# Kernel optimization log

Measured on AMD Instinct MI355X. Metric: run time of the kernel, lower is better.

## Reference

```python
import jax, jax.numpy as jnp
import numpy as np

B, T, C, H = 4, 2048, 1024, 16
D = C // H  # head_dim = 64

def setup_inputs() -> dict:
    key = jax.random.key(0)
    k1, k2, k3 = jax.random.split(key, 3)
    x = jax.random.normal(k1, (B, T, C), dtype=jnp.float32)
    w_qkv = jax.random.normal(k2, (C, 3 * C), dtype=jnp.float32) * (C ** -0.5)
    w_proj = jax.random.normal(k3, (C, C), dtype=jnp.float32) * (C ** -0.5)
    b_proj = jnp.zeros((C,), dtype=jnp.float32)
    return {"x": x, "w_qkv": w_qkv, "w_proj": w_proj, "b_proj": b_proj}

def reference(x, w_qkv, w_proj, b_proj):
    Bx, Tx, Cx = x.shape
    qkv = x @ w_qkv  # [B,T,3C]
    q, k, v = jnp.split(qkv, 3, axis=-1)
    # [B,T,H,D] -> [B,H,T,D]
    q = q.reshape(Bx, Tx, H, D).transpose(0, 2, 1, 3)
    k = k.reshape(Bx, Tx, H, D).transpose(0, 2, 1, 3)
    v = v.reshape(Bx, Tx, H, D).transpose(0, 2, 1, 3)
    scale = 1.0 / np.sqrt(D).astype(np.float32)
    att = jnp.einsum('bhqd,bhkd->bhqk', q, k) * scale  # [B,H,T,T]
    causal = jnp.tril(jnp.ones((Tx, Tx), dtype=bool))
    att = jnp.where(causal, att, -jnp.inf)
    att = jax.nn.softmax(att, axis=-1)
    y = jnp.einsum('bhqk,bhkd->bhqd', att, v)  # [B,H,T,D]
    y = y.transpose(0, 2, 1, 3).reshape(Bx, Tx, Cx)
    return y @ w_proj + b_proj
```

## Files before the change

### kernel.cpp

```cpp
#include <hip/hip_runtime.h>

typedef unsigned short u16;
typedef unsigned int u32;
typedef __attribute__((ext_vector_type(8))) short bf16x8;
typedef __attribute__((ext_vector_type(4))) float f32x4;
typedef __attribute__((ext_vector_type(16))) float f32x16;
typedef __attribute__((ext_vector_type(4))) unsigned short u16x4;

#define MFMA16(a, b, c) __builtin_amdgcn_mfma_f32_16x16x32_bf16((a), (b), (c), 0, 0, 0)
#define MFMA32(a, b, c) __builtin_amdgcn_mfma_f32_32x32x16_bf16((a), (b), (c), 0, 0, 0)

__device__ __forceinline__ u16 f2bf(float f) {
  union { float f; unsigned int i; } v; v.f = f;
  return (u16)((v.i + 0x7FFFu + ((v.i >> 16) & 1u)) >> 16);
}
__device__ __forceinline__ float exp2a(float x) {
  float r; asm("v_exp_f32 %0, %1" : "=v"(r) : "v"(x)); return r;
}
__device__ __forceinline__ u32 cvtpk(float lo, float hi) {
  u32 d; asm("v_cvt_pk_bf16_f32 %0, %1, %2" : "=v"(d) : "v"(lo), "v"(hi)); return d;
}
__device__ __forceinline__ void gl2lds16(const u16* g, u16* l) {
  __builtin_amdgcn_global_load_lds(
      (const __attribute__((address_space(1))) void*)g,
      (__attribute__((address_space(3))) void*)l, 16, 0, 0);
}

__global__ __launch_bounds__(256) void k_ingest(const float* __restrict__ src,
                                                u16* __restrict__ dst, int n8) {
  const int i = blockIdx.x * 256 + threadIdx.x;
  if (i >= n8) return;
  const float* s = src + (size_t)i * 8;
  float4 a = *(const float4*)(s);
  float4 b = *(const float4*)(s + 4);
  union { u16 o[8]; int4 v; } u;
  u.o[0] = f2bf(a.x); u.o[1] = f2bf(a.y); u.o[2] = f2bf(a.z); u.o[3] = f2bf(a.w);
  u.o[4] = f2bf(b.x); u.o[5] = f2bf(b.y); u.o[6] = f2bf(b.z); u.o[7] = f2bf(b.w);
  *(int4*)(&dst[(size_t)i * 8]) = u.v;
}

__global__ __launch_bounds__(256) void k_transpose(const float* __restrict__ src,
                                                   u16* __restrict__ dst, int R, int C) {
  __shared__ u16 tile[64][65];
  const int c0 = blockIdx.x * 64, r0 = blockIdx.y * 64;
  const int t = threadIdx.x;
#pragma unroll
  for (int i = 0; i < 16; ++i) {
    int e = i * 256 + t, rr = e >> 6, cc = e & 63;
    tile[rr][cc] = f2bf(src[(size_t)(r0 + rr) * C + c0 + cc]);
  }
  __syncthreads();
#pragma unroll
  for (int i = 0; i < 16; ++i) {
    int e = i * 256 + t, rr = e >> 6, cc = e & 63;
    dst[(size_t)(c0 + rr) * R + r0 + cc] = tile[cc][rr];
  }
}

template <int QKV>
__global__ __launch_bounds__(256) void k_gemm(
    const u16* __restrict__ A, const u16* __restrict__ Bt,
    const float* __restrict__ bias, float* __restrict__ Cf,
    u16* __restrict__ Qb, u16* __restrict__ Kb, u16* __restrict__ VTb,
    int M, int N, int K) {
  __shared__ __attribute__((aligned(16))) u16 As[128 * 32];
  __shared__ __attribute__((aligned(16))) u16 Bs[128 * 32];
  const int bn = blockIdx.x, bm = blockIdx.y;
  const int t = threadIdx.x, lane = t & 63, w = t >> 6;
  const int wr = w >> 1, wc = w & 1;
  const int rh = lane & 15, kg = lane >> 4;
  const int srow = lane >> 2, sk8 = (lane & 3) << 3;

  f32x4 acc[4][4];
#pragma unroll
  for (int mi = 0; mi < 4; ++mi)
#pragma unroll
    for (int ni = 0; ni < 4; ++ni) acc[mi][ni] = (f32x4)0.0f;

  for (int k0 = 0; k0 < K; k0 += 32) {
#pragma unroll
    for (int i = 0; i < 2; ++i) {
      const int r0 = w * 32 + i * 16;
      gl2lds16(&A[(size_t)(bm * 128 + r0 + srow) * K + k0 + sk8], &As[r0 * 32]);
      gl2lds16(&Bt[(size_t)(bn * 128 + r0 + srow) * K + k0 + sk8], &Bs[r0 * 32]);
    }
    asm volatile("s_waitcnt vmcnt(0)" ::: "memory");
    __syncthreads();

    bf16x8 af[4], bfr[4];
#pragma unroll
    for (int mi = 0; mi < 4; ++mi)
      af[mi] = *(const bf16x8*)(&As[(wr * 64 + mi * 16 + rh) * 32 + kg * 8]);
#pragma unroll
    for (int ni = 0; ni < 4; ++ni)
      bfr[ni] = *(const bf16x8*)(&Bs[(wc * 64 + ni * 16 + rh) * 32 + kg * 8]);
    __builtin_amdgcn_s_setprio(1);
#pragma unroll
    for (int mi = 0; mi < 4; ++mi)
#pragma unroll
      for (int ni = 0; ni < 4; ++ni)
        acc[mi][ni] = MFMA16(af[mi], bfr[ni], acc[mi][ni]);
    __builtin_amdgcn_s_setprio(0);
    __syncthreads();
  }

  if (QKV == 0) {
    const int rbase = bm * 128 + wr * 64;
    const int cbase = bn * 128 + wc * 64;
#pragma unroll
    for (int ni = 0; ni < 4; ++ni) {
      const int col = cbase + ni * 16 + rh;
      const float bv = bias ? bias[col] : 0.0f;
#pragma unroll
      for (int mi = 0; mi < 4; ++mi) {
#pragma unroll
        for (int r = 0; r < 4; ++r) {
          int row = rbase + mi * 16 + kg * 4 + r;
          Cf[(size_t)row * N + col] = acc[mi][ni][r] + bv;
        }
      }
    }
  } else {
    const float SCQ = 0.125f * 1.44269504f;
    const int rowbase = bm * 128 + wr * 64;
    const int b = rowbase >> 11;
    const int tb = rowbase & 2047;
    const int cbase = bn * 128 + wc * 64;
    const int role = cbase >> 10;
    const int h = (cbase & 1023) >> 6;
    const int bh = b * 16 + h;
#pragma unroll
    for (int ni = 0; ni < 4; ++ni) {
      const int d = ni * 16 + rh;
#pragma unroll
      for (int mi = 0; mi < 4; ++mi) {
        const int tt = tb + mi * 16 + kg * 4;
        if (role == 2) {
          u16x4 pk;
#pragma unroll
          for (int r = 0; r < 4; ++r) pk[r] = f2bf(acc[mi][ni][r]);
          *(u16x4*)(&VTb[((size_t)bh * 64 + d) * 2048 + tt]) = pk;
        } else {
          u16* dst = (role == 0) ? Qb : Kb;
          const float sc = (role == 0) ? SCQ : 1.0f;
#pragma unroll
          for (int r = 0; r < 4; ++r)
            dst[((size_t)bh * 2048 + tt + r) * 64 + d] = f2bf(acc[mi][ni][r] * sc);
        }
      }
    }
  }
}

__global__ __launch_bounds__(128, 2) void k_attn(const u16* __restrict__ Qb,
                                                 const u16* __restrict__ Kb,
                                                 const u16* __restrict__ VTb,
                                                 u16* __restrict__ Y) {
  const int bh = blockIdx.x;
  const int w = threadIdx.x >> 6;
  const int sb = w ? 31 - (int)blockIdx.y : (int)blockIdx.y;
  const int lane = threadIdx.x & 63;
  const int q31 = lane & 31, hi = lane >> 5;
  const int qA = sb * 64 + q31;
  const int qBr = sb * 64 + 32 + q31;
  const u16* Qh = Qb + (size_t)bh * 2048 * 64;
  const u16* Kh = Kb + (size_t)bh * 2048 * 64;
  const u16* Vh = VTb + (size_t)bh * 64 * 2048;
  const int b = bh >> 4, h = bh & 15;

  bf16x8 qfA[4], qfB[4];
#pragma unroll
  for (int d = 0; d < 4; ++d) {
    qfA[d] = *(const bf16x8*)(&Qh[(size_t)qA * 64 + d * 16 + hi * 8]);
    qfB[d] = *(const bf16x8*)(&Qh[(size_t)qBr * 64 + d * 16 + hi * 8]);
  }

  f32x16 oA0 = (f32x16)0.0f, oA1 = (f32x16)0.0f;
  f32x16 oB0 = (f32x16)0.0f, oB1 = (f32x16)0.0f;
  float mA = -1e30f, sA = 0.0f, mB = -1e30f, sB = 0.0f;

  const int nt = 2 * sb + 2;
  for (int tt = 0; tt < nt; ++tt) {
    const int j0 = tt * 32;
    const bool aAct = tt < nt - 1;

    bf16x8 kf[4];
#pragma unroll
    for (int d = 0; d < 4; ++d)
      kf[d] = *(const bf16x8*)(&Kh[(size_t)(j0 + q31) * 64 + d * 16 + hi * 8]);
    const bf16x8 vf0 = *(const bf16x8*)(&Vh[(size_t)q31 * 2048 + j0 + hi * 8]);
    const bf16x8 vf1 = *(const bf16x8*)(&Vh[(size_t)q31 * 2048 + j0 + 16 + hi * 8]);
    const bf16x8 vf2 = *(const bf16x8*)(&Vh[(size_t)(32 + q31) * 2048 + j0 + hi * 8]);
    const bf16x8 vf3 = *(const bf16x8*)(&Vh[(size_t)(32 + q31) * 2048 + j0 + 16 + hi * 8]);

    f32x16 stB = (f32x16)0.0f;
    __builtin_amdgcn_s_setprio(1);
#pragma unroll
    for (int d = 0; d < 4; ++d) stB = MFMA32(kf[d], qfB[d], stB);
    f32x16 stA = (f32x16)0.0f;
    if (aAct) {
#pragma unroll
      for (int d = 0; d < 4; ++d) stA = MFMA32(kf[d], qfA[d], stA);
    }
    __builtin_amdgcn_s_setprio(0);

    if (tt == nt - 2) {
#pragma unroll
      for (int r = 0; r < 16; ++r) {
        const int kcol = (r & 3) + 8 * (r >> 2) + 4 * hi;
        if (kcol > q31) stA[r] = -1e30f;
      }
    }
    if (tt == nt - 1) {
#pragma unroll
      for (int r = 0; r < 16; ++r) {
        const int kcol = (r & 3) + 8 * (r >> 2) + 4 * hi;
        if (kcol > q31) stB[r] = -1e30f;
      }
    }

    union { u32 w4[4]; bf16x8 f; } paA0, paA1, paB0, paB1;
    if (aAct) {
      float mx = fmaxf(
          fmaxf(fmaxf(fmaxf(stA[0], stA[1]), fmaxf(stA[2], stA[3])),
                fmaxf(fmaxf(stA[4], stA[5]), fmaxf(stA[6], stA[7]))),
          fmaxf(fmaxf(fmaxf(stA[8], stA[9]), fmaxf(stA[10], stA[11])),
                fmaxf(fmaxf(stA[12], stA[13]), fmaxf(stA[14], stA[15]))));
      if (__any(mx - mA > 8.0f)) {
        mx = fmaxf(mx, __shfl_xor(mx, 32));
        const float mn = fmaxf(mA, mx);
        const float scf = exp2a(mA - mn);
        mA = mn; sA *= scf; oA0 *= scf; oA1 *= scf;
      }
      float p[16];
#pragma unroll
      for (int r = 0; r < 16; ++r) p[r] = exp2a(stA[r] - mA);
      sA += (((p[0] + p[1]) + (p[2] + p[3])) + ((p[4] + p[5]) + (p[6] + p[7]))) +
            (((p[8] + p[9]) + (p[10] + p[11])) + ((p[12] + p[13]) + (p[14] + p[15])));
      u32 D0 = cvtpk(p[0], p[1]),   D1 = cvtpk(p[2], p[3]);
      u32 D2 = cvtpk(p[4], p[5]),   D3 = cvtpk(p[6], p[7]);
      u32 D4 = cvtpk(p[8], p[9]),   D5 = cvtpk(p[10], p[11]);
      u32 D6 = cvtpk(p[12], p[13]), D7 = cvtpk(p[14], p[15]);
      u32 X0 = __shfl_xor(D0, 32), X1 = __shfl_xor(D1, 32);
      u32 X2 = __shfl_xor(D2, 32), X3 = __shfl_xor(D3, 32);
      u32 X4 = __shfl_xor(D4, 32), X5 = __shfl_xor(D5, 32);
      u32 X6 = __shfl_xor(D6, 32), X7 = __shfl_xor(D7, 32);
      paA0.w4[0] = hi ? X2 : D0; paA0.w4[1] = hi ? X3 : D1;
      paA0.w4[2] = hi ? D2 : X0; paA0.w4[3] = hi ? D3 : X1;
      paA1.w4[0] = hi ? X6 : D4; paA1.w4[1] = hi ? X7 : D5;
      paA1.w4[2] = hi ? D6 : X4; paA1.w4[3] = hi ? D7 : X5;
    }

    {
      float mx = fmaxf(
          fmaxf(fmaxf(fmaxf(stB[0], stB[1]), fmaxf(stB[2], stB[3])),
                fmaxf(fmaxf(stB[4], stB[5]), fmaxf(stB[6], stB[7]))),
          fmaxf(fmaxf(fmaxf(stB[8], stB[9]), fmaxf(stB[10], stB[11])),
                fmaxf(fmaxf(stB[12], stB[13]), fmaxf(stB[14], stB[15]))));
      if (__any(mx - mB > 8.0f)) {
        mx = fmaxf(mx, __shfl_xor(mx, 32));
        const float mn = fmaxf(mB, mx);
        const float scf = exp2a(mB - mn);
        mB = mn; sB *= scf; oB0 *= scf; oB1 *= scf;
      }
      float p[16];
#pragma unroll
      for (int r = 0; r < 16; ++r) p[r] = exp2a(stB[r] - mB);
      sB += (((p[0] + p[1]) + (p[2] + p[3])) + ((p[4] + p[5]) + (p[6] + p[7]))) +
            (((p[8] + p[9]) + (p[10] + p[11])) + ((p[12] + p[13]) + (p[14] + p[15])));
      u32 D0 = cvtpk(p[0], p[1]),   D1 = cvtpk(p[2], p[3]);
      u32 D2 = cvtpk(p[4], p[5]),   D3 = cvtpk(p[6], p[7]);
      u32 D4 = cvtpk(p[8], p[9]),   D5 = cvtpk(p[10], p[11]);
      u32 D6 = cvtpk(p[12], p[13]), D7 = cvtpk(p[14], p[15]);
      u32 X0 = __shfl_xor(D0, 32), X1 = __shfl_xor(D1, 32);
      u32 X2 = __shfl_xor(D2, 32), X3 = __shfl_xor(D3, 32);
      u32 X4 = __shfl_xor(D4, 32), X5 = __shfl_xor(D5, 32);
      u32 X6 = __shfl_xor(D6, 32), X7 = __shfl_xor(D7, 32);
      paB0.w4[0] = hi ? X2 : D0; paB0.w4[1] = hi ? X3 : D1;
      paB0.w4[2] = hi ? D2 : X0; paB0.w4[3] = hi ? D3 : X1;
      paB1.w4[0] = hi ? X6 : D4; paB1.w4[1] = hi ? X7 : D5;
      paB1.w4[2] = hi ? D6 : X4; paB1.w4[3] = hi ? D7 : X5;
    }

    __builtin_amdgcn_s_setprio(1);
    oB0 = MFMA32(vf0, paB0.f, oB0);
    oB0 = MFMA32(vf1, paB1.f, oB0);
    oB1 = MFMA32(vf2, paB0.f, oB1);
    oB1 = MFMA32(vf3, paB1.f, oB1);
    if (aAct) {
      oA0 = MFMA32(vf0, paA0.f, oA0);
      oA0 = MFMA32(vf1, paA1.f, oA0);
      oA1 = MFMA32(vf2, paA0.f, oA1);
      oA1 = MFMA32(vf3, paA1.f, oA1);
    }
    __builtin_amdgcn_s_setprio(0);
  }

  sA += __shfl_xor(sA, 32);
  sB += __shfl_xor(sB, 32);
  const float invA = 1.0f / sA, invB = 1.0f / sB;
  u16* yrowA = Y + ((size_t)b * 2048 + qA) * 1024 + h * 64;
  u16* yrowB = Y + ((size_t)b * 2048 + qBr) * 1024 + h * 64;
#pragma unroll
  for (int a = 0; a < 4; ++a) {
    u16x4 pk;
#pragma unroll
    for (int i = 0; i < 4; ++i) pk[i] = f2bf(oA0[a * 4 + i] * invA);
    *(u16x4*)(yrowA + a * 8 + 4 * hi) = pk;
#pragma unroll
    for (int i = 0; i < 4; ++i) pk[i] = f2bf(oA1[a * 4 + i] * invA);
    *(u16x4*)(yrowA + 32 + a * 8 + 4 * hi) = pk;
#pragma unroll
    for (int i = 0; i < 4; ++i) pk[i] = f2bf(oB0[a * 4 + i] * invB);
    *(u16x4*)(yrowB + a * 8 + 4 * hi) = pk;
#pragma unroll
    for (int i = 0; i < 4; ++i) pk[i] = f2bf(oB1[a * 4 + i] * invB);
    *(u16x4*)(yrowB + 32 + a * 8 + 4 * hi) = pk;
  }
}

extern "C" void kernel_launch(void* const* d_in, const int* in_sizes, int n_in,
                              void* d_out, int out_size, void* d_ws, size_t ws_size,
                              hipStream_t stream) {
  const float* x      = (const float*)d_in[0];
  const float* w_qkv  = (const float*)d_in[1];
  const float* w_proj = (const float*)d_in[2];
  const float* b_proj = (const float*)d_in[3];
  float* out = (float*)d_out;

  char* ws = (char*)d_ws;
  u16* wqkvT  = (u16*)(ws);
  u16* wprojT = (u16*)(ws + 6291456);
  u16* Qb     = (u16*)(ws + 8388608);
  u16* Kb     = (u16*)(ws + 25165824);
  u16* VTb    = (u16*)(ws + 41943040);
  u16* xb     = (u16*)(ws + 58720256);
  u16* Yb     = xb;

  k_ingest<<<4096, 256, 0, stream>>>(x, xb, 1048576);
  k_transpose<<<dim3(48, 16), 256, 0, stream>>>(w_qkv, wqkvT, 1024, 3072);
  k_transpose<<<dim3(16, 16), 256, 0, stream>>>(w_proj, wprojT, 1024, 1024);
  k_gemm<1><<<dim3(24, 64), 256, 0, stream>>>(xb, wqkvT, nullptr, nullptr,
                                              Qb, Kb, VTb, 8192, 3072, 1024);
  k_attn<<<dim3(64, 16), 128, 0, stream>>>(Qb, Kb, VTb, Yb);
  k_gemm<0><<<dim3(8, 64), 256, 0, stream>>>(Yb, wprojT, b_proj, out,
                                             nullptr, nullptr, nullptr, 8192, 1024, 1024);
}
```

Measured before the change: 212.9 us.

## Split attention KV loop across two waves with LDS softmax merge

```diff
diff --git a/kernel.cpp b/kernel.cpp
--- a/kernel.cpp
+++ b/kernel.cpp
@@ -152,13 +152,14 @@
   }
 }
 
-__global__ __launch_bounds__(128, 2) void k_attn(const u16* __restrict__ Qb,
+__global__ __launch_bounds__(128, 4) void k_attn(const u16* __restrict__ Qb,
                                                  const u16* __restrict__ Kb,
                                                  const u16* __restrict__ VTb,
                                                  u16* __restrict__ Y) {
+  __shared__ float MG[64][68];
   const int bh = blockIdx.x;
+  const int sb = 31 - (int)blockIdx.y;
   const int w = threadIdx.x >> 6;
-  const int sb = w ? 31 - (int)blockIdx.y : (int)blockIdx.y;
   const int lane = threadIdx.x & 63;
   const int q31 = lane & 31, hi = lane >> 5;
   const int qA = sb * 64 + q31;
@@ -180,7 +181,7 @@
   float mA = -1e30f, sA = 0.0f, mB = -1e30f, sB = 0.0f;
 
   const int nt = 2 * sb + 2;
-  for (int tt = 0; tt < nt; ++tt) {
+  for (int tt = w; tt < nt; tt += 2) {
     const int j0 = tt * 32;
     const bool aAct = tt < nt - 1;
 
@@ -296,26 +297,60 @@
     __builtin_amdgcn_s_setprio(0);
   }
 
-  sA += __shfl_xor(sA, 32);
-  sB += __shfl_xor(sB, 32);
-  const float invA = 1.0f / sA, invB = 1.0f / sB;
-  u16* yrowA = Y + ((size_t)b * 2048 + qA) * 1024 + h * 64;
-  u16* yrowB = Y + ((size_t)b * 2048 + qBr) * 1024 + h * 64;
-#pragma unroll
-  for (int a = 0; a < 4; ++a) {
-    u16x4 pk;
-#pragma unroll
-    for (int i = 0; i < 4; ++i) pk[i] = f2bf(oA0[a * 4 + i] * invA);
-    *(u16x4*)(yrowA + a * 8 + 4 * hi) = pk;
-#pragma unroll
-    for (int i = 0; i < 4; ++i) pk[i] = f2bf(oA1[a * 4 + i] * invA);
-    *(u16x4*)(yrowA + 32 + a * 8 + 4 * hi) = pk;
-#pragma unroll
-    for (int i = 0; i < 4; ++i) pk[i] = f2bf(oB0[a * 4 + i] * invB);
-    *(u16x4*)(yrowB + a * 8 + 4 * hi) = pk;
-#pragma unroll
-    for (int i = 0; i < 4; ++i) pk[i] = f2bf(oB1[a * 4 + i] * invB);
-    *(u16x4*)(yrowB + 32 + a * 8 + 4 * hi) = pk;
+  if (w == 1) {
+    float* g = MG[lane];
+    g[0] = mA; g[1] = sA; g[2] = mB; g[3] = sB;
+#pragma unroll
+    for (int i = 0; i < 16; ++i) {
+      g[4 + i] = oA0[i]; g[20 + i] = oA1[i];
+      g[36 + i] = oB0[i]; g[52 + i] = oB1[i];
+    }
+  }
+  __syncthreads();
+  if (w == 0) {
+    const float* g = MG[lane];
+    u16* yrowA = Y + ((size_t)b * 2048 + qA) * 1024 + h * 64;
+    u16* yrowB = Y + ((size_t)b * 2048 + qBr) * 1024 + h * 64;
+    {
+      const float m1 = g[0], s1 = g[1];
+      const float mn = fmaxf(mA, m1);
+      const float fa = exp2a(mA - mn), fb = exp2a(m1 - mn);
+      float sm = sA * fa + s1 * fb;
+      sm += __shfl_xor(sm, 32);
+      const float inv = 1.0f / sm;
+#pragma unroll
+      for (int a = 0; a < 4; ++a) {
+        u16x4 pk;
+#pragma unroll
+        for (int i = 0; i < 4; ++i)
+          pk[i] = f2bf((oA0[a * 4 + i] * fa + g[4 + a * 4 + i] * fb) * inv);
+        *(u16x4*)(yrowA + a * 8 + 4 * hi) = pk;
+#pragma unroll
+        for (int i = 0; i < 4; ++i)
+          pk[i] = f2bf((oA1[a * 4 + i] * fa + g[20 + a * 4 + i] * fb) * inv);
+        *(u16x4*)(yrowA + 32 + a * 8 + 4 * hi) = pk;
+      }
+    }
+    {
+      const float m1 = g[2], s1 = g[3];
+      const float mn = fmaxf(mB, m1);
+      const float fa = exp2a(mB - mn), fb = exp2a(m1 - mn);
+      float sm = sB * fa + s1 * fb;
+      sm += __shfl_xor(sm, 32);
+      const float inv = 1.0f / sm;
+#pragma unroll
+      for (int a = 0; a < 4; ++a) {
+        u16x4 pk;
+#pragma unroll
+        for (int i = 0; i < 4; ++i)
+          pk[i] = f2bf((oB0[a * 4 + i] * fa + g[36 + a * 4 + i] * fb) * inv);
+        *(u16x4*)(yrowB + a * 8 + 4 * hi) = pk;
+#pragma unroll
+        for (int i = 0; i < 4; ++i)
+          pk[i] = f2bf((oB1[a * 4 + i] * fa + g[52 + a * 4 + i] * fb) * inv);
+        *(u16x4*)(yrowB + 32 + a * 8 + 4 * hi) = pk;
+      }
+    }
   }
 }
 
@@ -342,7 +377,7 @@
   k_transpose<<<dim3(16, 16), 256, 0, stream>>>(w_proj, wprojT, 1024, 1024);
   k_gemm<1><<<dim3(24, 64), 256, 0, stream>>>(xb, wqkvT, nullptr, nullptr,
                                               Qb, Kb, VTb, 8192, 3072, 1024);
-  k_attn<<<dim3(64, 16), 128, 0, stream>>>(Qb, Kb, VTb, Yb);
+  k_attn<<<dim3(64, 32), 128, 0, stream>>>(Qb, Kb, VTb, Yb);
   k_gemm<0><<<dim3(8, 64), 256, 0, stream>>>(Yb, wprojT, b_proj, out,
                                              nullptr, nullptr, nullptr, 8192, 1024, 1024);
 }
```

Result: slower. 391.8 us (+84.0%).
